# Kernel tuning notes

Hardware: AMD Instinct MI355X
Metric: run time of the kernel (lower is better)

The kernel has to match this reference:

```python
import jax, jax.numpy as jnp
import numpy as np

SEQ_LEN = 20          # hard-coded by the original module's 20x20 DataFrame
SCALE = 1e13          # mse() multiplies by 10000000000000
FRAME_SHAPE = (3, 720, 1280)


def setup_inputs() -> dict:
    key = jax.random.key(0)
    k1, k2 = jax.random.split(key)
    clip1 = jax.random.normal(k1, (SEQ_LEN,) + FRAME_SHAPE, dtype=jnp.float32)
    clip2 = jax.random.normal(k2, (SEQ_LEN,) + FRAME_SHAPE, dtype=jnp.float32)
    return {"clip1": clip1, "clip2": clip2}


def reference(clip1, clip2):
    # M[i, j] = -mean((clip1[j] - clip2[i])**2) * 1e13   (rows = clip2, cols = clip1)
    # Expand the squared difference: mean((a-b)^2) = mean(a^2) + mean(b^2) - 2*mean(a*b)
    # so we never materialize the [n, n, frame] difference tensor.
    n = clip1.shape[0]
    f = clip1[0].size
    c1 = clip1.reshape(n, -1)                       # [n, F]
    c2 = clip2.reshape(n, -1)                       # [n, F]
    m1 = jnp.mean(c1 * c1, axis=1)                  # [n] mean(clip1[j]^2)
    m2 = jnp.mean(c2 * c2, axis=1)                  # [n] mean(clip2[i]^2)
    cross = jnp.einsum('if,jf->ij', c2, c1) / f     # [n, n] mean(clip2[i]*clip1[j])
    M = -(m2[:, None] + m1[None, :] - 2.0 * cross) * SCALE

    # calculate_diagonals_partial: means of diagonals of M at offsets
    # k = -(n//2), ..., -1, 0, 1, ..., n//2 (offset = col - row),
    # each divided by its diagonal length (n - |k|), i.e. a mean.
    half = n // 2
    diags = [jnp.mean(jnp.diagonal(M, offset=k)) for k in range(-half, half + 1)]
    return jnp.stack(diags)                         # [n + 1] = [21]
```

## Files before the change

kernel.cpp:

```cpp
#include <hip/hip_runtime.h>
#include <hip/hip_bf16.h>

#define NN      20
#define FF      2764800
#define TK      64
#define NTILES  (FF / TK)
#define NBLK    1792
#define NTHREADS 256

typedef __attribute__((ext_vector_type(8))) short bf16x8;
typedef __attribute__((ext_vector_type(4))) float f32x4;


__global__ void zero_ws_kernel(float* __restrict__ ws, int n) {
    int i = blockIdx.x * blockDim.x + threadIdx.x;
    if (i < n) ws[i] = 0.0f;
}

static __device__ inline float sq4(float4 v) {
    return v.x * v.x + v.y * v.y + v.z * v.z + v.w * v.w;
}

static __device__ inline bf16x8 cvt8(float4 lo, float4 hi) {
    union { __hip_bfloat162 h[4]; bf16x8 v; } u;
    u.h[0] = __float22bfloat162_rn(float2{lo.x, lo.y});
    u.h[1] = __float22bfloat162_rn(float2{lo.z, lo.w});
    u.h[2] = __float22bfloat162_rn(float2{hi.x, hi.y});
    u.h[3] = __float22bfloat162_rn(float2{hi.z, hi.w});
    return u.v;
}

__global__ __launch_bounds__(NTHREADS, 7) void gram_kernel(
    const float* __restrict__ clip1,
    const float* __restrict__ clip2,
    float* __restrict__ ws,
    int repMask)
{
    __shared__ __align__(16) float s[2][40 * TK];

    const int tid  = threadIdx.x;
    const int lane = tid & 63;
    const int wv   = tid >> 6;
    const int sidx = lane & 15;
    const int kq   = lane >> 4;
    const int ti   = wv >> 1;
    const int tj   = wv & 1;

    const int nq = (wv < 2) ? 3 : 2;
    const float* gbase[3];
    unsigned voff[3];
    int lq[3];
    #pragma unroll
    for (int k = 0; k < 3; ++k) {
        int q   = wv + 4 * k;
        lq[k]   = q;
        int row = 4 * q + kq;
        int mm  = sidx ^ (row & 7);
        int rl  = (row < NN) ? row : row - NN;
        gbase[k] = (row < NN) ? clip2 : clip1;
        voff[k]  = (unsigned)rl * FF + (unsigned)mm * 4;
    }

    const int rowA = ti * 16 + sidx;
    const int rowB = 20 + tj * 16 + (tj ? (sidx < 4 ? sidx : 3) : sidx);
    const int swzA = rowA & 7;
    const int swzB = rowB & 7;

    f32x4 acc = {0.f, 0.f, 0.f, 0.f};
    float sqa = 0.f, sqb = 0.f;

    int t = blockIdx.x;
    #pragma unroll
    for (int k = 0; k < 3; ++k) {
        if (k < nq) {
            const float* ga = gbase[k] + (size_t)voff[k] + (size_t)t * TK;
            char* la = (char*)&s[0][0] + lq[k] * 1024;
            __builtin_amdgcn_global_load_lds(
                (const __attribute__((address_space(1))) void*)ga,
                (__attribute__((address_space(3))) void*)la, 16, 0, 0);
        }
    }
    __syncthreads();

    int cur = 0;
    while (t < NTILES) {
        const int tn = t + NBLK;
        if (tn < NTILES) {
            #pragma unroll
            for (int k = 0; k < 3; ++k) {
                if (k < nq) {
                    const float* ga = gbase[k] + (size_t)voff[k] + (size_t)tn * TK;
                    char* la = (char*)&s[cur ^ 1][0] + lq[k] * 1024;
                    __builtin_amdgcn_global_load_lds(
                        (const __attribute__((address_space(1))) void*)ga,
                        (__attribute__((address_space(3))) void*)la, 16, 0, 0);
                }
            }
        }

        const float* buf = &s[cur][0];
        #pragma unroll
        for (int ch = 0; ch < 2; ++ch) {
            const int bA = 8 * ch + 2 * kq;
            float4 a0 = *(const float4*)&buf[rowA * TK + (((bA    ) ^ swzA) << 2)];
            float4 a1 = *(const float4*)&buf[rowA * TK + (((bA + 1) ^ swzA) << 2)];
            float4 b0 = *(const float4*)&buf[rowB * TK + (((bA    ) ^ swzB) << 2)];
            float4 b1 = *(const float4*)&buf[rowB * TK + (((bA + 1) ^ swzB) << 2)];
            if (tj == 0) sqa += sq4(a0) + sq4(a1);
            if (ti == 0) sqb += sq4(b0) + sq4(b1);
            acc = __builtin_amdgcn_mfma_f32_16x16x32_bf16(
                      cvt8(a0, a1), cvt8(b0, b1), acc, 0, 0, 0);
        }

        __syncthreads();
        cur ^= 1;
        t = tn;
    }

    float* wsr = ws + (blockIdx.x & repMask) * 440;

    #pragma unroll
    for (int r = 0; r < 4; ++r) {
        int i = ti * 16 + kq * 4 + r;
        int j = tj * 16 + sidx;
        if (i < NN && j < NN) atomicAdd(&wsr[i * NN + j], acc[r]);
    }

    float va = sqa;
    va += __shfl_xor(va, 16);
    va += __shfl_xor(va, 32);
    if (tj == 0 && kq == 0) {
        int i = ti * 16 + sidx;
        if (i < NN) atomicAdd(&wsr[400 + i], va);
    }
    float vb = sqb;
    vb += __shfl_xor(vb, 16);
    vb += __shfl_xor(vb, 32);
    if (ti == 0 && kq == 0) {
        int j = tj * 16 + sidx;
        if (j < NN) atomicAdd(&wsr[420 + j], vb);
    }
}

__global__ void finalize_kernel(const float* __restrict__ ws, float* __restrict__ out,
                                int nrep) {
    __shared__ float w[440];
    const int tid = threadIdx.x;

    for (int e = tid; e < 440; e += 256) {
        float s = 0.0f;
        for (int rep = 0; rep < nrep; ++rep)
            s += ws[rep * 440 + e];
        w[e] = s;
    }
    __syncthreads();

    if (tid < 21) {
        int k  = tid - 10;
        int a  = k < 0 ? -k : k;
        int i0 = k < 0 ? -k : 0;
        int L  = NN - a;
        const float invF = 1.0f / (float)FF;
        float sum = 0.0f;
        for (int m = 0; m < L; ++m) {
            int i = i0 + m;
            int j = i + k;
            sum += w[400 + i] + w[420 + j] - 2.0f * w[i * NN + j];
        }
        out[tid] = -(sum * invF / (float)L) * 1e13f;
    }
}

extern "C" void kernel_launch(void* const* d_in, const int* in_sizes, int n_in,
                              void* d_out, int out_size, void* d_ws, size_t ws_size,
                              hipStream_t stream) {
    const float* clip1 = (const float*)d_in[0];
    const float* clip2 = (const float*)d_in[1];
    float* out = (float*)d_out;
    float* ws  = (float*)d_ws;

    int nrep = 1;
    while (nrep < 64 && (size_t)(nrep * 2) * 440 * sizeof(float) <= ws_size)
        nrep *= 2;

    int nz = nrep * 440;
    zero_ws_kernel<<<(nz + 255) / 256, 256, 0, stream>>>(ws, nz);
    gram_kernel<<<NBLK, NTHREADS, 0, stream>>>(clip1, clip2, ws, nrep - 1);
    finalize_kernel<<<1, 256, 0, stream>>>(ws, out, nrep);
}
```

Baseline: 131.1 us.

## Enlarge K-tile to 256 with 8-wave blocks, split-K waves, and vmcnt-based pipelining

Raises the K tile from 64 to 256 columns and uses 512-thread blocks in which two wave groups split the K range. The grid shrinks to 512 blocks. Each wave now stages 5 full rows through direct-to-LDS loads, and explicit vmcnt waits with raw s_barrier replace __syncthreads so the next tile's loads overlap compute. Squared norms move to a per-row pass over LDS with a full wave reduction. The intent is to cut per-tile barrier and issue overhead and to deepen memory overlap, at the cost of more LDS per block (80KB double-buffered) and fewer resident blocks.

Result: faster. 120.4 us (median of 2 runs) (-8.2%).

```diff
diff --git a/kernel.cpp b/kernel.cpp
--- a/kernel.cpp
+++ b/kernel.cpp
@@ -3,10 +3,11 @@
 
 #define NN      20
 #define FF      2764800
-#define TK      64
+#define TK      256
+#define NROWS   40
 #define NTILES  (FF / TK)
-#define NBLK    1792
-#define NTHREADS 256
+#define NBLK    512
+#define NTHREADS 512
 
 typedef __attribute__((ext_vector_type(8))) short bf16x8;
 typedef __attribute__((ext_vector_type(4))) float f32x4;
@@ -15,10 +16,6 @@
 __global__ void zero_ws_kernel(float* __restrict__ ws, int n) {
     int i = blockIdx.x * blockDim.x + threadIdx.x;
     if (i < n) ws[i] = 0.0f;
-}
-
-static __device__ inline float sq4(float4 v) {
-    return v.x * v.x + v.y * v.y + v.z * v.z + v.w * v.w;
 }
 
 static __device__ inline bf16x8 cvt8(float4 lo, float4 hi) {
@@ -30,36 +27,44 @@
     return u.v;
 }
 
-__global__ __launch_bounds__(NTHREADS, 7) void gram_kernel(
+__global__ __launch_bounds__(NTHREADS, 4) void gram_kernel(
     const float* __restrict__ clip1,
     const float* __restrict__ clip2,
     float* __restrict__ ws,
     int repMask)
 {
-    __shared__ __align__(16) float s[2][40 * TK];
+    __shared__ __align__(16) float s[2][NROWS * TK];
 
     const int tid  = threadIdx.x;
     const int lane = tid & 63;
     const int wv   = tid >> 6;
     const int sidx = lane & 15;
     const int kq   = lane >> 4;
-    const int ti   = wv >> 1;
     const int tj   = wv & 1;
+    const int ti   = (wv >> 1) & 1;
+    const int kh   = wv >> 2;
 
-    const int nq = (wv < 2) ? 3 : 2;
-    const float* gbase[3];
-    unsigned voff[3];
-    int lq[3];
+    const float* srcp[5];
+    int ldsoff[5];
     #pragma unroll
-    for (int k = 0; k < 3; ++k) {
-        int q   = wv + 4 * k;
-        lq[k]   = q;
-        int row = 4 * q + kq;
-        int mm  = sidx ^ (row & 7);
-        int rl  = (row < NN) ? row : row - NN;
-        gbase[k] = (row < NN) ? clip2 : clip1;
-        voff[k]  = (unsigned)rl * FF + (unsigned)mm * 4;
+    for (int ss = 0; ss < 5; ++ss) {
+        int r = 5 * wv + ss;
+        const float* base = (r < NN) ? (clip2 + (size_t)r * FF)
+                                     : (clip1 + (size_t)(r - NN) * FF);
+        srcp[ss]   = base + ((lane ^ (r & 7)) << 2);
+        ldsoff[ss] = r * (TK * 4);
     }
+
+    auto stage = [&](int bi, int tile) {
+        #pragma unroll
+        for (int ss = 0; ss < 5; ++ss) {
+            const float* ga = srcp[ss] + (size_t)tile * TK;
+            char* la = (char*)&s[bi][0] + ldsoff[ss];
+            __builtin_amdgcn_global_load_lds(
+                (const __attribute__((address_space(1))) void*)ga,
+                (__attribute__((address_space(3))) void*)la, 16, 0, 0);
+        }
+    };
 
     const int rowA = ti * 16 + sidx;
     const int rowB = 20 + tj * 16 + (tj ? (sidx < 4 ? sidx : 3) : sidx);
@@ -67,52 +72,42 @@
     const int swzB = rowB & 7;
 
     f32x4 acc = {0.f, 0.f, 0.f, 0.f};
-    float sqa = 0.f, sqb = 0.f;
+    float sqr[5] = {0.f, 0.f, 0.f, 0.f, 0.f};
 
     int t = blockIdx.x;
-    #pragma unroll
-    for (int k = 0; k < 3; ++k) {
-        if (k < nq) {
-            const float* ga = gbase[k] + (size_t)voff[k] + (size_t)t * TK;
-            char* la = (char*)&s[0][0] + lq[k] * 1024;
-            __builtin_amdgcn_global_load_lds(
-                (const __attribute__((address_space(1))) void*)ga,
-                (__attribute__((address_space(3))) void*)la, 16, 0, 0);
-        }
-    }
-    __syncthreads();
+    stage(0, t);
+    int cur = 0;
 
-    int cur = 0;
     while (t < NTILES) {
         const int tn = t + NBLK;
         if (tn < NTILES) {
-            #pragma unroll
-            for (int k = 0; k < 3; ++k) {
-                if (k < nq) {
-                    const float* ga = gbase[k] + (size_t)voff[k] + (size_t)tn * TK;
-                    char* la = (char*)&s[cur ^ 1][0] + lq[k] * 1024;
-                    __builtin_amdgcn_global_load_lds(
-                        (const __attribute__((address_space(1))) void*)ga,
-                        (__attribute__((address_space(3))) void*)la, 16, 0, 0);
-                }
-            }
+            stage(cur ^ 1, tn);
+            asm volatile("s_waitcnt vmcnt(5)" ::: "memory");
+        } else {
+            asm volatile("s_waitcnt vmcnt(0)" ::: "memory");
         }
+        __builtin_amdgcn_sched_barrier(0);
+        __builtin_amdgcn_s_barrier();
 
         const float* buf = &s[cur][0];
         #pragma unroll
-        for (int ch = 0; ch < 2; ++ch) {
-            const int bA = 8 * ch + 2 * kq;
+        for (int m = 0; m < 4; ++m) {
+            const int k0 = kh * 128 + 32 * m;
+            const int bA = (k0 >> 2) + 2 * kq;
             float4 a0 = *(const float4*)&buf[rowA * TK + (((bA    ) ^ swzA) << 2)];
             float4 a1 = *(const float4*)&buf[rowA * TK + (((bA + 1) ^ swzA) << 2)];
             float4 b0 = *(const float4*)&buf[rowB * TK + (((bA    ) ^ swzB) << 2)];
             float4 b1 = *(const float4*)&buf[rowB * TK + (((bA + 1) ^ swzB) << 2)];
-            if (tj == 0) sqa += sq4(a0) + sq4(a1);
-            if (ti == 0) sqb += sq4(b0) + sq4(b1);
             acc = __builtin_amdgcn_mfma_f32_16x16x32_bf16(
                       cvt8(a0, a1), cvt8(b0, b1), acc, 0, 0, 0);
         }
+        #pragma unroll
+        for (int ss = 0; ss < 5; ++ss) {
+            float4 v = *(const float4*)&buf[(5 * wv + ss) * TK + (lane << 2)];
+            sqr[ss] += v.x * v.x + v.y * v.y + v.z * v.z + v.w * v.w;
+        }
 
-        __syncthreads();
+        __builtin_amdgcn_s_barrier();
         cur ^= 1;
         t = tn;
     }
@@ -126,19 +121,16 @@
         if (i < NN && j < NN) atomicAdd(&wsr[i * NN + j], acc[r]);
     }
 
-    float va = sqa;
-    va += __shfl_xor(va, 16);
-    va += __shfl_xor(va, 32);
-    if (tj == 0 && kq == 0) {
-        int i = ti * 16 + sidx;
-        if (i < NN) atomicAdd(&wsr[400 + i], va);
-    }
-    float vb = sqb;
-    vb += __shfl_xor(vb, 16);
-    vb += __shfl_xor(vb, 32);
-    if (ti == 0 && kq == 0) {
-        int j = tj * 16 + sidx;
-        if (j < NN) atomicAdd(&wsr[420 + j], vb);
+    #pragma unroll
+    for (int ss = 0; ss < 5; ++ss) {
+        float vq = sqr[ss];
+        vq += __shfl_xor(vq, 32);
+        vq += __shfl_xor(vq, 16);
+        vq += __shfl_xor(vq, 8);
+        vq += __shfl_xor(vq, 4);
+        vq += __shfl_xor(vq, 2);
+        vq += __shfl_xor(vq, 1);
+        if (lane == 0) atomicAdd(&wsr[400 + 5 * wv + ss], vq);
     }
 }
 
```
